# Kernel tuning notes

Measured on AMD Instinct MI355X. Metric: run time of the kernel, lower is better.

The kernel has to match this reference:

```python
import jax, jax.numpy as jnp
import numpy as np

N_ING, N_TASTE, E, D = 100000, 50000, 600000, 128
NEG_SLOPE = 0.2  # HANConv default negative_slope


def setup_inputs() -> dict:
    key = jax.random.key(0)
    ks = jax.random.split(key, 10)
    s = 1.0 / np.sqrt(D)
    return {
        "x_ing": jax.random.normal(ks[0], (N_ING, D), jnp.float32),
        "x_taste": jax.random.normal(ks[1], (N_TASTE, D), jnp.float32),
        "src": jax.random.randint(ks[2], (E,), 0, N_ING, dtype=jnp.int32),
        "dst": jax.random.randint(ks[3], (E,), 0, N_TASTE, dtype=jnp.int32),
        "W_ing": jax.random.normal(ks[4], (D, D), jnp.float32) * s,
        "b_ing": jnp.zeros((D,), jnp.float32),
        "W_taste": jax.random.normal(ks[5], (D, D), jnp.float32) * s,
        "b_taste": jnp.zeros((D,), jnp.float32),
        "att_src": jax.random.normal(ks[6], (D,), jnp.float32) * s,
        "att_dst": jax.random.normal(ks[7], (D,), jnp.float32) * s,
        "W_k": jax.random.normal(ks[8], (D, D), jnp.float32) * s,
        "b_k": jnp.zeros((D,), jnp.float32),
        "q": jax.random.normal(ks[9], (D,), jnp.float32) * s,
    }


def reference(x_ing, x_taste, src, dst, W_ing, b_ing, W_taste, b_taste,
              att_src, att_dst, W_k, b_k, q):
    # --- HANConv node-type projections (heads=1, so view is identity) ---
    h_src = x_ing @ W_ing + b_ing      # [N_ING, D]
    h_dst = x_taste @ W_taste + b_taste  # [N_TASTE, D]

    # --- per-edge-type GAT-style attention on ('ingredient','part_of','taste') ---
    a_src = h_src @ att_src            # [N_ING]
    a_dst = h_dst @ att_dst            # [N_TASTE]
    alpha = jax.nn.leaky_relu(a_src[src] + a_dst[dst], NEG_SLOPE)  # [E]

    # segment softmax over incoming edges of each taste node (PyG softmax)
    amax = jax.ops.segment_max(alpha, dst, num_segments=N_TASTE)   # [N_TASTE]
    e = jnp.exp(alpha - amax[dst])
    denom = jax.ops.segment_sum(e, dst, num_segments=N_TASTE)
    w = e / (denom[dst] + 1e-16)       # [E]  (dropout=identity in eval)

    # weighted message aggregation + ReLU (HANConv applies relu post-propagate)
    msg = h_src[src] * w[:, None]      # [E, D]  dominant memory traffic
    agg = jax.ops.segment_sum(msg, dst, num_segments=N_TASTE)      # [N_TASTE, D]
    out = jax.nn.relu(agg)

    # --- semantic-level attention (single edge type -> beta == 1) ---
    score = jnp.sum(q * jnp.tanh(out @ W_k + b_k).mean(axis=0))    # scalar
    beta = jax.nn.softmax(score[None])[0]                          # == 1.0
    out = beta * out

    # --- TasteGNN wrapper: restore ingredient, residual on taste ---
    taste = out + x_taste
    return (x_ing, taste)
```

## Files before the change

kernel.cpp:

```cpp
#include <hip/hip_runtime.h>
#include <math.h>

#define N_ING 100000
#define N_TASTE 50000
#define D 128
#define NEG_SLOPE 0.2f

typedef float nt4 __attribute__((ext_vector_type(4)));

__global__ __launch_bounds__(128) void k_prep(const float* __restrict__ W_taste,
                                              const float* __restrict__ b_taste,
                                              const float* __restrict__ att_dst,
                                              float* __restrict__ v_dst,
                                              float* __restrict__ c_dst) {
  __shared__ float red[128];
  const int t = threadIdx.x;
  float acc = 0.f;
  const float* row = W_taste + t * D;
  for (int d = 0; d < D; d += 4) {
    float4 w = *(const float4*)(row + d);
    float4 a = *(const float4*)(att_dst + d);
    acc += w.x * a.x + w.y * a.y + w.z * a.z + w.w * a.w;
  }
  v_dst[t] = acc;
  red[t] = b_taste[t] * att_dst[t];
  __syncthreads();
  for (int off = 64; off > 0; off >>= 1) {
    if (t < off) red[t] += red[t + off];
    __syncthreads();
  }
  if (t == 0) *c_dst = red[0];
}

__global__ __launch_bounds__(256) void k_gemm(const float* __restrict__ X,
                                              const float* __restrict__ W,
                                              const float* __restrict__ bias,
                                              const float* __restrict__ att,
                                              float* __restrict__ H,
                                              float* __restrict__ a_src,
                                              float* __restrict__ pass_out) {
  __shared__ __align__(16) float Xt[32 * 132];
  __shared__ __align__(16) float Wl[16 * 260];
  const int tid = threadIdx.x;
  const int tr = tid >> 4, tc = tid & 15;
  const int r0 = tr * 8, c0 = tc * 8;
  const int brow = blockIdx.x * 128;

  float acc[8][8];
#pragma unroll
  for (int i = 0; i < 8; ++i)
#pragma unroll
    for (int j = 0; j < 8; ++j) acc[i][j] = 0.f;

  for (int k0 = 0; k0 < D; k0 += 32) {
#pragma unroll
    for (int p = 0; p < 4; ++p) {
      int f = p * 256 + tid;
      int kk = f >> 5;
      int j4 = f & 31;
      float4 w4 = *(const float4*)(W + (size_t)(k0 + kk) * D + j4 * 4);
      int g = j4 >> 1;
      int u0 = (j4 & 1) * 4;
      *(float4*)&Wl[g * 260 + kk * 8 + u0] = w4;
    }
#pragma unroll
    for (int p = 0; p < 4; ++p) {
      int f = p * 256 + tid;
      int r = f >> 3;
      int kq = (f & 7) * 4;
      int row = brow + r;
      float4 x4 = make_float4(0.f, 0.f, 0.f, 0.f);
      if (row < N_ING) {
        x4 = *(const float4*)(X + (size_t)row * D + k0 + kq);
        if (pass_out)
          __builtin_nontemporal_store(*(const nt4*)&x4,
              (nt4*)(pass_out + (size_t)row * D + k0 + kq));
      }
      Xt[(kq + 0) * 132 + r] = x4.x;
      Xt[(kq + 1) * 132 + r] = x4.y;
      Xt[(kq + 2) * 132 + r] = x4.z;
      Xt[(kq + 3) * 132 + r] = x4.w;
    }
    __syncthreads();
#pragma unroll 4
    for (int kk = 0; kk < 32; ++kk) {
      float xa[8], wb[8];
      *(float4*)&xa[0] = *(const float4*)&Xt[kk * 132 + r0];
      *(float4*)&xa[4] = *(const float4*)&Xt[kk * 132 + r0 + 4];
      *(float4*)&wb[0] = *(const float4*)&Wl[tc * 260 + kk * 8];
      *(float4*)&wb[4] = *(const float4*)&Wl[tc * 260 + kk * 8 + 4];
#pragma unroll
      for (int i = 0; i < 8; ++i)
#pragma unroll
        for (int j = 0; j < 8; ++j) acc[i][j] = fmaf(xa[i], wb[j], acc[i][j]);
    }
    __syncthreads();
  }

  float bj[8], av[8];
  *(float4*)&bj[0] = *(const float4*)(bias + c0);
  *(float4*)&bj[4] = *(const float4*)(bias + c0 + 4);
  *(float4*)&av[0] = *(const float4*)(att + c0);
  *(float4*)&av[4] = *(const float4*)(att + c0 + 4);
#pragma unroll
  for (int i = 0; i < 8; ++i) {
    int row = brow + r0 + i;
    if (row < N_ING) {
      float o[8];
      float part = 0.f;
#pragma unroll
      for (int j = 0; j < 8; ++j) {
        o[j] = acc[i][j] + bj[j];
        part += o[j] * av[j];
      }
      *(float4*)(H + (size_t)row * D + c0) = *(float4*)&o[0];
      *(float4*)(H + (size_t)row * D + c0 + 4) = *(float4*)&o[4];
      part += __shfl_xor(part, 1);
      part += __shfl_xor(part, 2);
      part += __shfl_xor(part, 4);
      part += __shfl_xor(part, 8);
      if (tc == 0) a_src[row] = part;
    }
  }
}

__global__ __launch_bounds__(256) void k_hist(const int* __restrict__ dst,
                                              int* __restrict__ count, int E) {
  int e = blockIdx.x * 256 + threadIdx.x;
  if (e < E) atomicAdd(&count[dst[e]], 1);
}

__global__ __launch_bounds__(256) void k_scan1(const int* __restrict__ count,
                                               int* __restrict__ excl,
                                               int* __restrict__ bsum, int n) {
  __shared__ int tmp[256];
  const int tid = threadIdx.x;
  const int i = blockIdx.x * 256 + tid;
  int v = (i < n) ? count[i] : 0;
  tmp[tid] = v;
  __syncthreads();
  for (int off = 1; off < 256; off <<= 1) {
    int a = tmp[tid];
    int b = (tid >= off) ? tmp[tid - off] : 0;
    __syncthreads();
    tmp[tid] = a + b;
    __syncthreads();
  }
  if (i < n) excl[i] = tmp[tid] - v;
  if (tid == 255) bsum[blockIdx.x] = tmp[255];
}

__global__ __launch_bounds__(256) void k_scan2(int* __restrict__ bsum, int nb) {
  __shared__ int tmp[256];
  const int tid = threadIdx.x;
  int v = (tid < nb) ? bsum[tid] : 0;
  tmp[tid] = v;
  __syncthreads();
  for (int off = 1; off < 256; off <<= 1) {
    int a = tmp[tid];
    int b = (tid >= off) ? tmp[tid - off] : 0;
    __syncthreads();
    tmp[tid] = a + b;
    __syncthreads();
  }
  if (tid < nb) bsum[tid] = tmp[tid] - v;
}

__global__ __launch_bounds__(256) void k_scan3(const int* __restrict__ excl,
                                               const int* __restrict__ bsum,
                                               int* __restrict__ offsets,
                                               int* __restrict__ cursor,
                                               int n, int E) {
  const int i = blockIdx.x * 256 + threadIdx.x;
  if (i < n) {
    int o = excl[i] + bsum[blockIdx.x];
    offsets[i] = o;
    cursor[i] = o;
  }
  if (i == 0) offsets[n] = E;
}

__global__ __launch_bounds__(256) void k_scatter(const int* __restrict__ src,
                                                 const int* __restrict__ dst,
                                                 const float* __restrict__ a_src,
                                                 int* __restrict__ cursor,
                                                 int2* __restrict__ csr_pack,
                                                 int E) {
  int e = blockIdx.x * 256 + threadIdx.x;
  if (e < E) {
    int s = src[e];
    float a = a_src[s];
    int pos = atomicAdd(&cursor[dst[e]], 1);
    csr_pack[pos] = make_int2(s, __float_as_int(a));
  }
}

__global__ __launch_bounds__(256) void k_agg(const int* __restrict__ offsets,
                                             const int2* __restrict__ csr_pack,
                                             const float* __restrict__ v_dst,
                                             const float* __restrict__ c_dst,
                                             const float* __restrict__ H,
                                             const float* __restrict__ x_taste,
                                             float* __restrict__ out_taste) {
  const int wid = threadIdx.x >> 6, lane = threadIdx.x & 63;
  const int n = blockIdx.x * 4 + wid;
  const int d = lane * 2;

  const int o0 = offsets[n], o1 = offsets[n + 1];
  const int cnt = o1 - o0;
  const bool fast = (cnt <= 64);

  int2 pk = make_int2(0, 0);
  if (fast && lane < cnt) pk = csr_pack[o0 + lane];
  const int s_l = pk.x;
  const float a_s = __int_as_float(pk.y);

  const float2 xt2 = *(const float2*)(x_taste + (size_t)n * D + d);
  const float2 v2 = *(const float2*)(v_dst + d);
  float adn = xt2.x * v2.x + xt2.y * v2.y;
#pragma unroll
  for (int off = 1; off < 64; off <<= 1) adn += __shfl_xor(adn, off);
  adn += *c_dst;

  float denom = 0.f;
  float2 acc0 = make_float2(0.f, 0.f);
  float2 acc1 = make_float2(0.f, 0.f);
  float2 acc2 = make_float2(0.f, 0.f);
  float2 acc3 = make_float2(0.f, 0.f);

  if (fast) {
    float al_l = -INFINITY;
    if (lane < cnt) {
      float al = a_s + adn;
      al_l = al >= 0.f ? al : NEG_SLOPE * al;
    }
    float am = al_l;
#pragma unroll
    for (int off = 1; off < 64; off <<= 1) am = fmaxf(am, __shfl_xor(am, off));
    float ev_l = (lane < cnt) ? __expf(al_l - am) : 0.f;
    float es = ev_l;
#pragma unroll
    for (int off = 1; off < 64; off <<= 1) es += __shfl_xor(es, off);
    denom = es;
    int e = 0;
    for (; e + 4 <= cnt; e += 4) {
      int s0 = __shfl(s_l, e);
      int s1 = __shfl(s_l, e + 1);
      int s2 = __shfl(s_l, e + 2);
      int s3 = __shfl(s_l, e + 3);
      float ev0 = __shfl(ev_l, e);
      float ev1 = __shfl(ev_l, e + 1);
      float ev2 = __shfl(ev_l, e + 2);
      float ev3 = __shfl(ev_l, e + 3);
      const float2 h0 = *(const float2*)(H + (size_t)s0 * D + d);
      const float2 h1 = *(const float2*)(H + (size_t)s1 * D + d);
      const float2 h2 = *(const float2*)(H + (size_t)s2 * D + d);
      const float2 h3 = *(const float2*)(H + (size_t)s3 * D + d);
      acc0.x = fmaf(ev0, h0.x, acc0.x);
      acc0.y = fmaf(ev0, h0.y, acc0.y);
      acc1.x = fmaf(ev1, h1.x, acc1.x);
      acc1.y = fmaf(ev1, h1.y, acc1.y);
      acc2.x = fmaf(ev2, h2.x, acc2.x);
      acc2.y = fmaf(ev2, h2.y, acc2.y);
      acc3.x = fmaf(ev3, h3.x, acc3.x);
      acc3.y = fmaf(ev3, h3.y, acc3.y);
    }
    for (; e < cnt; ++e) {
      int s0 = __shfl(s_l, e);
      float ev0 = __shfl(ev_l, e);
      const float2 h0 = *(const float2*)(H + (size_t)s0 * D + d);
      acc0.x = fmaf(ev0, h0.x, acc0.x);
      acc0.y = fmaf(ev0, h0.y, acc0.y);
    }
  } else {
    float am = -INFINITY;
    for (int i = o0 + lane; i < o1; i += 64) {
      float al = __int_as_float(csr_pack[i].y) + adn;
      al = al >= 0.f ? al : NEG_SLOPE * al;
      am = fmaxf(am, al);
    }
#pragma unroll
    for (int off = 1; off < 64; off <<= 1) am = fmaxf(am, __shfl_xor(am, off));
    for (int base = 0; base < cnt; base += 64) {
      int m = min(64, cnt - base);
      int s_t = 0;
      float ev_t = 0.f;
      if (lane < m) {
        int2 p = csr_pack[o0 + base + lane];
        s_t = p.x;
        float al = __int_as_float(p.y) + adn;
        al = al >= 0.f ? al : NEG_SLOPE * al;
        ev_t = __expf(al - am);
      }
      float es = ev_t;
#pragma unroll
      for (int off = 1; off < 64; off <<= 1) es += __shfl_xor(es, off);
      denom += es;
      int e = 0;
      for (; e + 2 <= m; e += 2) {
        int s0 = __shfl(s_t, e);
        int s1 = __shfl(s_t, e + 1);
        float ev0 = __shfl(ev_t, e);
        float ev1 = __shfl(ev_t, e + 1);
        const float2 h0 = *(const float2*)(H + (size_t)s0 * D + d);
        const float2 h1 = *(const float2*)(H + (size_t)s1 * D + d);
        acc0.x = fmaf(ev0, h0.x, acc0.x);
        acc0.y = fmaf(ev0, h0.y, acc0.y);
        acc1.x = fmaf(ev1, h1.x, acc1.x);
        acc1.y = fmaf(ev1, h1.y, acc1.y);
      }
      if (e < m) {
        int s0 = __shfl(s_t, e);
        float ev0 = __shfl(ev_t, e);
        const float2 h0 = *(const float2*)(H + (size_t)s0 * D + d);
        acc0.x = fmaf(ev0, h0.x, acc0.x);
        acc0.y = fmaf(ev0, h0.y, acc0.y);
      }
    }
  }

  const float inv = 1.f / (denom + 1e-16f);
  float2 r;
  r.x = fmaxf((acc0.x + acc1.x + acc2.x + acc3.x) * inv, 0.f) + xt2.x;
  r.y = fmaxf((acc0.y + acc1.y + acc2.y + acc3.y) * inv, 0.f) + xt2.y;
  *(float2*)(out_taste + (size_t)n * D + d) = r;
}

extern "C" void kernel_launch(void* const* d_in, const int* in_sizes, int n_in,
                              void* d_out, int out_size, void* d_ws, size_t ws_size,
                              hipStream_t stream) {
  const float* x_ing   = (const float*)d_in[0];
  const float* x_taste = (const float*)d_in[1];
  const int*   src     = (const int*)d_in[2];
  const int*   dst     = (const int*)d_in[3];
  const float* W_ing   = (const float*)d_in[4];
  const float* b_ing   = (const float*)d_in[5];
  const float* W_taste = (const float*)d_in[6];
  const float* b_taste = (const float*)d_in[7];
  const float* att_src = (const float*)d_in[8];
  const float* att_dst = (const float*)d_in[9];
  const int E = in_sizes[2];

  float* out_ing   = (float*)d_out;
  float* out_taste = (float*)d_out + (size_t)N_ING * D;

  size_t off = 0;
  auto alloc = [&](size_t bytes) -> void* {
    void* p = (char*)d_ws + off;
    off = (off + bytes + 255) & ~(size_t)255;
    return p;
  };
  float* a_src    = (float*)alloc((size_t)N_ING * 4);
  float* v_dst    = (float*)alloc(D * 4);
  float* c_dst    = (float*)alloc(4);
  int* count      = (int*)alloc((size_t)N_TASTE * 4);
  int* excl       = (int*)alloc((size_t)N_TASTE * 4);
  int* bsum       = (int*)alloc(256 * 4);
  int* offsets    = (int*)alloc((size_t)(N_TASTE + 1) * 4);
  int* cursor     = (int*)alloc((size_t)N_TASTE * 4);
  int2* csr_pack  = (int2*)alloc((size_t)E * 8);
  float* H_ws     = (float*)alloc((size_t)N_ING * D * 4);
  const bool h_in_ws = (off <= ws_size);

  float* H = h_in_ws ? H_ws : out_ing;

  const int nb_node = (N_TASTE + 255) / 256;
  const int nb_edge = (E + 255) / 256;

  (void)hipMemsetAsync(count, 0, (size_t)N_TASTE * 4, stream);
  k_prep<<<1, 128, 0, stream>>>(W_taste, b_taste, att_dst, v_dst, c_dst);
  k_hist<<<nb_edge, 256, 0, stream>>>(dst, count, E);
  k_scan1<<<nb_node, 256, 0, stream>>>(count, excl, bsum, N_TASTE);
  k_scan2<<<1, 256, 0, stream>>>(bsum, nb_node);
  k_scan3<<<nb_node, 256, 0, stream>>>(excl, bsum, offsets, cursor, N_TASTE, E);
  k_gemm<<<(N_ING + 127) / 128, 256, 0, stream>>>(x_ing, W_ing, b_ing, att_src,
                                                  H, a_src,
                                                  h_in_ws ? out_ing : nullptr);
  k_scatter<<<nb_edge, 256, 0, stream>>>(src, dst, a_src, cursor, csr_pack, E);
  k_agg<<<N_TASTE / 4, 256, 0, stream>>>(offsets, csr_pack, v_dst, c_dst,
                                         H, x_taste, out_taste);
  if (!h_in_ws) {
    (void)hipMemcpyAsync(d_out, x_ing, (size_t)N_ING * D * 4,
                         hipMemcpyDeviceToDevice, stream);
  }
}
```

Baseline: 320.6 us.

## Hold full W in LDS and stream X rows into registers in GEMM

Result: slower. 335.1 us (+4.5%).

```diff
diff --git a/kernel.cpp b/kernel.cpp
--- a/kernel.cpp
+++ b/kernel.cpp
@@ -5,8 +5,6 @@
 #define N_TASTE 50000
 #define D 128
 #define NEG_SLOPE 0.2f
-
-typedef float nt4 __attribute__((ext_vector_type(4)));
 
 __global__ __launch_bounds__(128) void k_prep(const float* __restrict__ W_taste,
                                               const float* __restrict__ b_taste,
@@ -32,69 +30,59 @@
   if (t == 0) *c_dst = red[0];
 }
 
-__global__ __launch_bounds__(256) void k_gemm(const float* __restrict__ X,
-                                              const float* __restrict__ W,
-                                              const float* __restrict__ bias,
-                                              const float* __restrict__ att,
-                                              float* __restrict__ H,
-                                              float* __restrict__ a_src,
-                                              float* __restrict__ pass_out) {
-  __shared__ __align__(16) float Xt[32 * 132];
-  __shared__ __align__(16) float Wl[16 * 260];
+__global__ __launch_bounds__(256, 2) void k_gemm(const float* __restrict__ X,
+                                                 const float* __restrict__ W,
+                                                 const float* __restrict__ bias,
+                                                 const float* __restrict__ att,
+                                                 float* __restrict__ H,
+                                                 float* __restrict__ a_src) {
+  __shared__ __align__(16) float Wl[16 * 1028];
   const int tid = threadIdx.x;
   const int tr = tid >> 4, tc = tid & 15;
   const int r0 = tr * 8, c0 = tc * 8;
   const int brow = blockIdx.x * 128;
 
+#pragma unroll
+  for (int p = 0; p < 16; ++p) {
+    int f = p * 256 + tid;
+    int kk = f >> 5;
+    int j4 = f & 31;
+    float4 w4 = *(const float4*)(W + (size_t)kk * D + j4 * 4);
+    *(float4*)&Wl[(j4 >> 1) * 1028 + kk * 8 + (j4 & 1) * 4] = w4;
+  }
+  __syncthreads();
+
   float acc[8][8];
 #pragma unroll
   for (int i = 0; i < 8; ++i)
 #pragma unroll
     for (int j = 0; j < 8; ++j) acc[i][j] = 0.f;
 
-  for (int k0 = 0; k0 < D; k0 += 32) {
-#pragma unroll
-    for (int p = 0; p < 4; ++p) {
-      int f = p * 256 + tid;
-      int kk = f >> 5;
-      int j4 = f & 31;
-      float4 w4 = *(const float4*)(W + (size_t)(k0 + kk) * D + j4 * 4);
-      int g = j4 >> 1;
-      int u0 = (j4 & 1) * 4;
-      *(float4*)&Wl[g * 260 + kk * 8 + u0] = w4;
-    }
-#pragma unroll
-    for (int p = 0; p < 4; ++p) {
-      int f = p * 256 + tid;
-      int r = f >> 3;
-      int kq = (f & 7) * 4;
-      int row = brow + r;
-      float4 x4 = make_float4(0.f, 0.f, 0.f, 0.f);
-      if (row < N_ING) {
-        x4 = *(const float4*)(X + (size_t)row * D + k0 + kq);
-        if (pass_out)
-          __builtin_nontemporal_store(*(const nt4*)&x4,
-              (nt4*)(pass_out + (size_t)row * D + k0 + kq));
-      }
-      Xt[(kq + 0) * 132 + r] = x4.x;
-      Xt[(kq + 1) * 132 + r] = x4.y;
-      Xt[(kq + 2) * 132 + r] = x4.z;
-      Xt[(kq + 3) * 132 + r] = x4.w;
-    }
-    __syncthreads();
-#pragma unroll 4
-    for (int kk = 0; kk < 32; ++kk) {
-      float xa[8], wb[8];
-      *(float4*)&xa[0] = *(const float4*)&Xt[kk * 132 + r0];
-      *(float4*)&xa[4] = *(const float4*)&Xt[kk * 132 + r0 + 4];
-      *(float4*)&wb[0] = *(const float4*)&Wl[tc * 260 + kk * 8];
-      *(float4*)&wb[4] = *(const float4*)&Wl[tc * 260 + kk * 8 + 4];
-#pragma unroll
-      for (int i = 0; i < 8; ++i)
-#pragma unroll
-        for (int j = 0; j < 8; ++j) acc[i][j] = fmaf(xa[i], wb[j], acc[i][j]);
-    }
-    __syncthreads();
+  int rows[8];
+#pragma unroll
+  for (int i = 0; i < 8; ++i) {
+    int r = brow + r0 + i;
+    rows[i] = r < N_ING ? r : N_ING - 1;
+  }
+
+  for (int kk4 = 0; kk4 < 32; ++kk4) {
+    float4 xr[8];
+#pragma unroll
+    for (int i = 0; i < 8; ++i)
+      xr[i] = *(const float4*)(X + (size_t)rows[i] * D + kk4 * 4);
+#pragma unroll
+    for (int u = 0; u < 4; ++u) {
+      int kk = kk4 * 4 + u;
+      float wb[8];
+      *(float4*)&wb[0] = *(const float4*)&Wl[tc * 1028 + kk * 8];
+      *(float4*)&wb[4] = *(const float4*)&Wl[tc * 1028 + kk * 8 + 4];
+#pragma unroll
+      for (int i = 0; i < 8; ++i) {
+        float xs = (&xr[i].x)[u];
+#pragma unroll
+        for (int j = 0; j < 8; ++j) acc[i][j] = fmaf(xs, wb[j], acc[i][j]);
+      }
+    }
   }
 
   float bj[8], av[8];
@@ -368,14 +356,17 @@
   const int nb_edge = (E + 255) / 256;
 
   (void)hipMemsetAsync(count, 0, (size_t)N_TASTE * 4, stream);
+  if (h_in_ws) {
+    (void)hipMemcpyAsync(out_ing, x_ing, (size_t)N_ING * D * 4,
+                         hipMemcpyDeviceToDevice, stream);
+  }
   k_prep<<<1, 128, 0, stream>>>(W_taste, b_taste, att_dst, v_dst, c_dst);
   k_hist<<<nb_edge, 256, 0, stream>>>(dst, count, E);
   k_scan1<<<nb_node, 256, 0, stream>>>(count, excl, bsum, N_TASTE);
   k_scan2<<<1, 256, 0, stream>>>(bsum, nb_node);
   k_scan3<<<nb_node, 256, 0, stream>>>(excl, bsum, offsets, cursor, N_TASTE, E);
   k_gemm<<<(N_ING + 127) / 128, 256, 0, stream>>>(x_ing, W_ing, b_ing, att_src,
-                                                  H, a_src,
-                                                  h_in_ws ? out_ing : nullptr);
+                                                  H, a_src);
   k_scatter<<<nb_edge, 256, 0, stream>>>(src, dst, a_src, cursor, csr_pack, E);
   k_agg<<<N_TASTE / 4, 256, 0, stream>>>(offsets, csr_pack, v_dst, c_dst,
                                          H, x_taste, out_taste);
```
